# Kernel tuning notes

Hardware: AMD Instinct MI355X
Metric: run time of the kernel (lower is better)

## Reference

```python
import jax, jax.numpy as jnp
import numpy as np

DIM = 1024
NUM_HEADS = 16
HEAD_DIM = DIM // NUM_HEADS
SCALE = 1.0 / float(np.sqrt(HEAD_DIM))


def setup_inputs() -> dict:
    key = jax.random.key(0)
    ks = jax.random.split(key, 5)
    B, S = 2, 2048
    x = jax.random.normal(ks[0], (B, S, DIM), dtype=jnp.float32)
    qkv_w = jax.random.normal(ks[1], (3 * DIM, DIM), dtype=jnp.float32) * (1.0 / np.sqrt(DIM))
    qkv_b = jax.random.normal(ks[2], (3 * DIM,), dtype=jnp.float32) * 0.02
    proj_w = jax.random.normal(ks[3], (DIM, DIM), dtype=jnp.float32) * (1.0 / np.sqrt(DIM))
    proj_b = jax.random.normal(ks[4], (DIM,), dtype=jnp.float32) * 0.02
    return {"x": x, "qkv_w": qkv_w, "qkv_b": qkv_b, "proj_w": proj_w, "proj_b": proj_b}


def reference(x, qkv_w, qkv_b, proj_w, proj_b):
    B, S, _ = x.shape
    # qkv projection: (B,S,3*DIM) -> (3, B, H, S, Dh)
    qkv = x @ qkv_w.T + qkv_b
    qkv = qkv.reshape(B, S, 3, NUM_HEADS, HEAD_DIM).transpose(2, 0, 3, 1, 4)
    q, k, v = qkv[0], qkv[1], qkv[2]
    # scaled dot-product attention (full score matrix, as in the original)
    scores = jnp.einsum('bhqd,bhkd->bhqk', q, k) * SCALE
    attn = jax.nn.softmax(scores, axis=-1)
    out = jnp.einsum('bhqk,bhkd->bhqd', attn, v)  # (B,H,S,Dh)
    out = out.transpose(0, 2, 1, 3).reshape(B, S, DIM)
    return out @ proj_w.T + proj_b
```

## Files before the change

kernel.cpp:

```cpp
#include <hip/hip_runtime.h>

#define DIM_ 1024
#define NH_ 16
#define HD_ 64
#define B_ 2
#define S_ 2048
#define M_ (B_ * S_)
#define NQKV_ (3 * DIM_)

typedef __attribute__((ext_vector_type(8))) __bf16 bf16x8;
typedef __attribute__((ext_vector_type(4))) __bf16 bf16x4;
typedef __attribute__((ext_vector_type(4))) float f32x4;

__device__ __forceinline__ void gl_lds16(const void* g, void* l) {
  __builtin_amdgcn_global_load_lds(
      (__attribute__((address_space(1))) void*)const_cast<void*>(g),
      (__attribute__((address_space(3))) void*)l, 16, 0, 0);
}

#define N4_X 1048576
#define N4_W1 786432
#define N4_W2 262144
__global__ __launch_bounds__(256) void cast_all(const float* __restrict__ x,
                                                const float* __restrict__ w1,
                                                const float* __restrict__ w2,
                                                __bf16* __restrict__ xb,
                                                __bf16* __restrict__ w1b,
                                                __bf16* __restrict__ w2b) {
  int i = blockIdx.x * 256 + threadIdx.x;
  const int stride = gridDim.x * 256;
  for (; i < N4_X + N4_W1 + N4_W2; i += stride) {
    const float4* src;
    bf16x4* dst;
    int j;
    if (i < N4_X) { src = (const float4*)x; dst = (bf16x4*)xb; j = i; }
    else if (i < N4_X + N4_W1) { src = (const float4*)w1; dst = (bf16x4*)w1b; j = i - N4_X; }
    else { src = (const float4*)w2; dst = (bf16x4*)w2b; j = i - (N4_X + N4_W1); }
    float4 v = src[j];
    bf16x4 o;
    o[0] = (__bf16)v.x; o[1] = (__bf16)v.y; o[2] = (__bf16)v.z; o[3] = (__bf16)v.w;
    dst[j] = o;
  }
}

template <int MODE, int BM>
__global__ __launch_bounds__(512, 4) void gemm_bt(const __bf16* __restrict__ A,
                                                  const __bf16* __restrict__ Bw,
                                                  const float* __restrict__ bias,
                                                  __bf16* __restrict__ Qp, __bf16* __restrict__ Kp,
                                                  __bf16* __restrict__ Vt,
                                                  float* __restrict__ Cout) {
  constexpr int KD = 1024;
  constexpr int BN = 128;
  constexpr int MT = BM / 64;
  constexpr int NC = (BM + BN) / 64;
  __shared__ __bf16 As[BM * 64];
  __shared__ __bf16 Bs[BN * 64];
  const int tid = threadIdx.x;
  const int lane = tid & 63;
  const int wave = tid >> 6;
  const int quad = lane >> 4;
  const int r16 = lane & 15;
  const int wm = wave >> 1;
  const int wn = wave & 1;
  const int m0 = blockIdx.y * BM;
  const int n0 = blockIdx.x * BN;

  const f32x4 fz = {0.f, 0.f, 0.f, 0.f};
  f32x4 acc[MT][4];
#pragma unroll
  for (int i = 0; i < MT; ++i)
#pragma unroll
    for (int j = 0; j < 4; ++j) acc[i][j] = fz;

  const __bf16* gp[NC];
  __bf16* lp[NC];
#pragma unroll
  for (int i = 0; i < NC; ++i) {
    const int c = tid + i * 512;
    if (c < BM * 8) {
      const int r = c >> 3, cc = c & 7;
      gp[i] = A + (size_t)(m0 + r) * KD + ((cc ^ (r & 7)) * 8);
      lp[i] = &As[c * 8];
    } else {
      const int c2 = c - BM * 8;
      const int r = c2 >> 3, cc = c2 & 7;
      gp[i] = Bw + (size_t)(n0 + r) * KD + ((cc ^ (r & 7)) * 8);
      lp[i] = &Bs[c2 * 8];
    }
  }

  for (int kt = 0; kt < KD / 64; ++kt) {
    __syncthreads();
#pragma unroll
    for (int i = 0; i < NC; ++i) { gl_lds16(gp[i], lp[i]); gp[i] += 64; }
    __syncthreads();

#pragma unroll
    for (int sub = 0; sub < 2; ++sub) {
      const int ch = ((sub * 4 + quad) ^ (r16 & 7)) * 8;
      bf16x8 af[MT], bfr[4];
#pragma unroll
      for (int mt = 0; mt < MT; ++mt)
        af[mt] = *(const bf16x8*)&As[(wm * MT * 16 + mt * 16 + r16) * 64 + ch];
#pragma unroll
      for (int nt = 0; nt < 4; ++nt)
        bfr[nt] = *(const bf16x8*)&Bs[(wn * 64 + nt * 16 + r16) * 64 + ch];
#pragma unroll
      for (int mt = 0; mt < MT; ++mt)
#pragma unroll
        for (int nt = 0; nt < 4; ++nt)
          acc[mt][nt] =
              __builtin_amdgcn_mfma_f32_16x16x32_bf16(af[mt], bfr[nt], acc[mt][nt], 0, 0, 0);
    }
  }

  if (MODE == 0) {
#pragma unroll
    for (int nt = 0; nt < 4; ++nt) {
      const int n = n0 + wn * 64 + nt * 16 + r16;
      const int sel = n >> 10;
      const int h = (n >> 6) & 15;
      const int dh = n & 63;
      const float bs = bias[n];
      if (sel == 2) {
#pragma unroll
        for (int mt = 0; mt < MT; ++mt) {
          const int m = m0 + wm * MT * 16 + mt * 16 + quad * 4;
          const int b = m >> 11;
          const int s = m & 2047;
          const int slot = (s & ~31) | (((s >> 2) & 3) << 3) | (((s >> 4) & 1) << 2);
          bf16x4 ov;
#pragma unroll
          for (int r = 0; r < 4; ++r) ov[r] = (__bf16)(acc[mt][nt][r] + bs);
          *(bf16x4*)&Vt[((size_t)((b * NH_ + h) * HD_ + dh)) * S_ + slot] = ov;
        }
      } else {
        __bf16* dst = (sel == 0) ? Qp : Kp;
        const float mul = (sel == 0) ? 0.18033688011112042f : 1.0f;
#pragma unroll
        for (int mt = 0; mt < MT; ++mt) {
#pragma unroll
          for (int r = 0; r < 4; ++r) {
            const int m = m0 + wm * MT * 16 + mt * 16 + quad * 4 + r;
            const int b = m >> 11;
            const int s = m & 2047;
            dst[((size_t)((b * NH_ + h) * S_ + s)) * HD_ + dh] =
                (__bf16)((acc[mt][nt][r] + bs) * mul);
          }
        }
      }
    }
  } else {
#pragma unroll
    for (int nt = 0; nt < 4; ++nt) {
      const int n = n0 + wn * 64 + nt * 16 + r16;
      const float bs = bias[n];
#pragma unroll
      for (int mt = 0; mt < MT; ++mt) {
#pragma unroll
        for (int r = 0; r < 4; ++r) {
          const int m = m0 + wm * MT * 16 + mt * 16 + quad * 4 + r;
          Cout[(size_t)m * DIM_ + n] = acc[mt][nt][r] + bs;
        }
      }
    }
  }
}

__global__ __launch_bounds__(512, 4) void attn(const __bf16* __restrict__ Qp,
                                               const __bf16* __restrict__ Kp,
                                               const __bf16* __restrict__ Vtp,
                                               __bf16* __restrict__ ctx) {
  __shared__ __bf16 smem[2][2][2][64 * 64];
  const int tid = threadIdx.x;
  const int lane = tid & 63;
  const int wave = tid >> 6;
  const int quad = lane >> 4;
  const int r16 = lane & 15;
  const int qg = wave & 3;
  const int kh = wave >> 2;
  const int bh = blockIdx.y;
  const int q0 = blockIdx.x * 128;

  bf16x8 qf[2][2];
#pragma unroll
  for (int g = 0; g < 2; ++g) {
    const __bf16* qb = Qp + ((size_t)bh * S_ + q0 + qg * 32 + g * 16 + r16) * HD_;
    qf[g][0] = *(const bf16x8*)(qb + quad * 8);
    qf[g][1] = *(const bf16x8*)(qb + 32 + quad * 8);
  }

  const f32x4 fz = {0.f, 0.f, 0.f, 0.f};
  f32x4 o[2][4];
  float lsum[2] = {0.f, 0.f};
#pragma unroll
  for (int g = 0; g < 2; ++g)
#pragma unroll
    for (int d = 0; d < 4; ++d) o[g][d] = fz;

  const __bf16* gp[4];
  int gstep[4], lkv[4], lhh[4], lof[4];
#pragma unroll
  for (int i = 0; i < 4; ++i) {
    const int c = tid + i * 512;
    if (c < 1024) {
      const int hh = c >> 9, c2 = c & 511;
      const int kr = c2 >> 3, kc = c2 & 7;
      gp[i] = Kp + ((size_t)bh * S_ + hh * 1024 + kr) * HD_ + ((kc ^ (kr & 7)) * 8);
      gstep[i] = 64 * HD_;
      lkv[i] = 0; lhh[i] = hh; lof[i] = c2 * 8;
    } else {
      const int c1 = c - 1024;
      const int hh = c1 >> 9, c2 = c1 & 511;
      const int vr = c2 >> 3, vc = c2 & 7;
      gp[i] = Vtp + ((size_t)bh * HD_ + vr) * S_ + hh * 1024 + ((vc ^ (vr & 7)) * 8);
      gstep[i] = 64;
      lkv[i] = 1; lhh[i] = hh; lof[i] = c2 * 8;
    }
  }

#pragma unroll
  for (int i = 0; i < 4; ++i) {
    gl_lds16(gp[i], &smem[0][lkv[i]][lhh[i]][lof[i]]);
    gp[i] += gstep[i];
  }

  for (int kt = 0; kt < 16; ++kt) {
    const int cb = kt & 1;
    __syncthreads();
    if (kt + 1 < 16) {
#pragma unroll
      for (int i = 0; i < 4; ++i) {
        gl_lds16(gp[i], &smem[cb ^ 1][lkv[i]][lhh[i]][lof[i]]);
        gp[i] += gstep[i];
      }
    }

    const __bf16* Kt = &smem[cb][0][kh][0];
    const __bf16* Vt2 = &smem[cb][1][kh][0];
#pragma unroll
    for (int ks = 0; ks < 2; ++ks) {
      f32x4 sa[2][2];
#pragma unroll
      for (int mt2 = 0; mt2 < 2; ++mt2) {
        const int row = (ks * 2 + mt2) * 16 + r16;
        bf16x8 k0 = *(const bf16x8*)&Kt[row * 64 + ((quad ^ (row & 7)) * 8)];
        bf16x8 k1 = *(const bf16x8*)&Kt[row * 64 + (((4 + quad) ^ (row & 7)) * 8)];
#pragma unroll
        for (int g = 0; g < 2; ++g) {
          f32x4 t = fz;
          t = __builtin_amdgcn_mfma_f32_16x16x32_bf16(k0, qf[g][0], t, 0, 0, 0);
          t = __builtin_amdgcn_mfma_f32_16x16x32_bf16(k1, qf[g][1], t, 0, 0, 0);
          sa[mt2][g] = t;
        }
      }

      bf16x8 pf[2];
#pragma unroll
      for (int g = 0; g < 2; ++g)
#pragma unroll
        for (int r = 0; r < 4; ++r) {
          float p0 = __builtin_amdgcn_exp2f(sa[0][g][r]);
          float p1 = __builtin_amdgcn_exp2f(sa[1][g][r]);
          lsum[g] += p0 + p1;
          pf[g][r] = (__bf16)p0;
          pf[g][4 + r] = (__bf16)p1;
        }

#pragma unroll
      for (int dt = 0; dt < 4; ++dt) {
        const int row = dt * 16 + r16;
        bf16x8 va = *(const bf16x8*)&Vt2[row * 64 + (((ks * 4 + quad) ^ (row & 7)) * 8)];
#pragma unroll
        for (int g = 0; g < 2; ++g)
          o[g][dt] = __builtin_amdgcn_mfma_f32_16x16x32_bf16(va, pf[g], o[g][dt], 0, 0, 0);
      }
    }
  }

#pragma unroll
  for (int g = 0; g < 2; ++g) {
    lsum[g] += __shfl_xor(lsum[g], 16);
    lsum[g] += __shfl_xor(lsum[g], 32);
  }

  float* xch = (float*)smem;
  __syncthreads();
  if (kh == 1) {
#pragma unroll
    for (int g = 0; g < 2; ++g) {
#pragma unroll
      for (int dt = 0; dt < 4; ++dt)
        *(f32x4*)&xch[(qg * 8 + g * 4 + dt) * 256 + lane * 4] = o[g][dt];
      xch[8192 + qg * 128 + g * 64 + lane] = lsum[g];
    }
  }
  __syncthreads();
  if (kh == 0) {
    const int b = bh >> 4, h = bh & 15;
#pragma unroll
    for (int g = 0; g < 2; ++g) {
      const float l = lsum[g] + xch[8192 + qg * 128 + g * 64 + lane];
      const float inv = 1.0f / l;
      const int s = q0 + qg * 32 + g * 16 + r16;
#pragma unroll
      for (int dt = 0; dt < 4; ++dt) {
        f32x4 op = *(const f32x4*)&xch[(qg * 8 + g * 4 + dt) * 256 + lane * 4];
        bf16x4 ov;
#pragma unroll
        for (int r = 0; r < 4; ++r) ov[r] = (__bf16)((o[g][dt][r] + op[r]) * inv);
        *(bf16x4*)&ctx[((size_t)(b * S_ + s)) * DIM_ + h * 64 + dt * 16 + quad * 4] = ov;
      }
    }
  }
}

extern "C" void kernel_launch(void* const* d_in, const int* in_sizes, int n_in, void* d_out,
                              int out_size, void* d_ws, size_t ws_size, hipStream_t stream) {
  const float* x = (const float*)d_in[0];
  const float* qkv_w = (const float*)d_in[1];
  const float* qkv_b = (const float*)d_in[2];
  const float* proj_w = (const float*)d_in[3];
  const float* proj_b = (const float*)d_in[4];
  float* out = (float*)d_out;

  char* ws = (char*)d_ws;
  __bf16* Xb = (__bf16*)(ws);
  __bf16* Wb = (__bf16*)(ws + 8388608);
  __bf16* Pb = (__bf16*)(ws + 14680064);
  __bf16* Qp = (__bf16*)(ws + 16777216);
  __bf16* Kp = (__bf16*)(ws + 25165824);
  __bf16* Vt = (__bf16*)(ws + 33554432);
  __bf16* Cx = (__bf16*)(ws + 41943040);

  cast_all<<<2048, 256, 0, stream>>>(x, qkv_w, proj_w, Xb, Wb, Pb);
  gemm_bt<0, 128><<<dim3(NQKV_ / 128, M_ / 128), 512, 0, stream>>>(Xb, Wb, qkv_b, Qp, Kp, Vt,
                                                                   nullptr);
  attn<<<dim3(S_ / 128, 32), 512, 0, stream>>>(Qp, Kp, Vt, Cx);
  gemm_bt<1, 64><<<dim3(DIM_ / 128, M_ / 64), 512, 0, stream>>>(Cx, Pb, proj_b, nullptr, nullptr,
                                                                nullptr, out);
}
```

Measured before the change: 173.9 us.

## Split attention keys across four wave groups with 1024-thread blocks

The attention kernel now runs 1024 threads per block. Four key-split wave groups each handle 32 keys of a 128-key tile, and partial outputs are combined through a two-stage LDS reduction. The grid is reordered so that blockIdx.x indexes batch-head, which changes the block scheduling order and possibly L2 reuse. The aim is to cut the serial loop work per wave and the global-to-LDS load count per thread. The cost is a larger 70 KB LDS footprint, fewer resident blocks per CU, and extra reduction synchronisation.

```diff
diff --git a/kernel.cpp b/kernel.cpp
--- a/kernel.cpp
+++ b/kernel.cpp
@@ -168,11 +168,16 @@
   }
 }
 
-__global__ __launch_bounds__(512, 4) void attn(const __bf16* __restrict__ Qp,
-                                               const __bf16* __restrict__ Kp,
-                                               const __bf16* __restrict__ Vtp,
-                                               __bf16* __restrict__ ctx) {
-  __shared__ __bf16 smem[2][2][2][64 * 64];
+__global__ __launch_bounds__(1024, 8) void attn(const __bf16* __restrict__ Qp,
+                                                const __bf16* __restrict__ Kp,
+                                                const __bf16* __restrict__ Vtp,
+                                                __bf16* __restrict__ ctx) {
+  __shared__ __align__(16) char smem_raw[71680];
+  __bf16* Ks = (__bf16*)smem_raw;
+  __bf16* Vs = (__bf16*)(smem_raw + 32768);
+  float* xch = (float*)smem_raw;
+  float* lx = (float*)(smem_raw + 69632);
+
   const int tid = threadIdx.x;
   const int lane = tid & 63;
   const int wave = tid >> 6;
@@ -180,8 +185,8 @@
   const int r16 = lane & 15;
   const int qg = wave & 3;
   const int kh = wave >> 2;
-  const int bh = blockIdx.y;
-  const int q0 = blockIdx.x * 128;
+  const int bh = blockIdx.x;
+  const int q0 = blockIdx.y * 128;
 
   bf16x8 qf[2][2];
 #pragma unroll
@@ -199,83 +204,60 @@
 #pragma unroll
     for (int d = 0; d < 4; ++d) o[g][d] = fz;
 
-  const __bf16* gp[4];
-  int gstep[4], lkv[4], lhh[4], lof[4];
-#pragma unroll
-  for (int i = 0; i < 4; ++i) {
-    const int c = tid + i * 512;
-    if (c < 1024) {
-      const int hh = c >> 9, c2 = c & 511;
-      const int kr = c2 >> 3, kc = c2 & 7;
-      gp[i] = Kp + ((size_t)bh * S_ + hh * 1024 + kr) * HD_ + ((kc ^ (kr & 7)) * 8);
-      gstep[i] = 64 * HD_;
-      lkv[i] = 0; lhh[i] = hh; lof[i] = c2 * 8;
-    } else {
-      const int c1 = c - 1024;
-      const int hh = c1 >> 9, c2 = c1 & 511;
-      const int vr = c2 >> 3, vc = c2 & 7;
-      gp[i] = Vtp + ((size_t)bh * HD_ + vr) * S_ + hh * 1024 + ((vc ^ (vr & 7)) * 8);
-      gstep[i] = 64;
-      lkv[i] = 1; lhh[i] = hh; lof[i] = c2 * 8;
-    }
-  }
-
-#pragma unroll
-  for (int i = 0; i < 4; ++i) {
-    gl_lds16(gp[i], &smem[0][lkv[i]][lhh[i]][lof[i]]);
-    gp[i] += gstep[i];
-  }
+  const int krow = tid >> 3, kcol = tid & 7;
+  const __bf16* gk = Kp + ((size_t)bh * S_ + krow) * HD_ + ((kcol ^ (krow & 7)) * 8);
+  const int kof = tid * 8;
+  const int vrow = tid >> 4, vcol = tid & 15;
+  const __bf16* gv = Vtp + ((size_t)bh * HD_ + vrow) * S_ + ((vcol ^ (vrow & 15)) * 8);
+  const int vof = tid * 8;
+
+  gl_lds16(gk, &Ks[kof]); gk += 128 * HD_;
+  gl_lds16(gv, &Vs[vof]); gv += 128;
 
   for (int kt = 0; kt < 16; ++kt) {
     const int cb = kt & 1;
     __syncthreads();
     if (kt + 1 < 16) {
-#pragma unroll
-      for (int i = 0; i < 4; ++i) {
-        gl_lds16(gp[i], &smem[cb ^ 1][lkv[i]][lhh[i]][lof[i]]);
-        gp[i] += gstep[i];
-      }
-    }
-
-    const __bf16* Kt = &smem[cb][0][kh][0];
-    const __bf16* Vt2 = &smem[cb][1][kh][0];
-#pragma unroll
-    for (int ks = 0; ks < 2; ++ks) {
-      f32x4 sa[2][2];
-#pragma unroll
-      for (int mt2 = 0; mt2 < 2; ++mt2) {
-        const int row = (ks * 2 + mt2) * 16 + r16;
-        bf16x8 k0 = *(const bf16x8*)&Kt[row * 64 + ((quad ^ (row & 7)) * 8)];
-        bf16x8 k1 = *(const bf16x8*)&Kt[row * 64 + (((4 + quad) ^ (row & 7)) * 8)];
-#pragma unroll
-        for (int g = 0; g < 2; ++g) {
-          f32x4 t = fz;
-          t = __builtin_amdgcn_mfma_f32_16x16x32_bf16(k0, qf[g][0], t, 0, 0, 0);
-          t = __builtin_amdgcn_mfma_f32_16x16x32_bf16(k1, qf[g][1], t, 0, 0, 0);
-          sa[mt2][g] = t;
-        }
-      }
-
-      bf16x8 pf[2];
+      gl_lds16(gk, &Ks[(cb ^ 1) * 8192 + kof]); gk += 128 * HD_;
+      gl_lds16(gv, &Vs[(cb ^ 1) * 8192 + vof]); gv += 128;
+    }
+    const __bf16* Kt = &Ks[cb * 8192];
+    const __bf16* Vt2 = &Vs[cb * 8192];
+
+    f32x4 sa[2][2];
+#pragma unroll
+    for (int mt2 = 0; mt2 < 2; ++mt2) {
+      const int row = kh * 32 + mt2 * 16 + r16;
+      bf16x8 k0 = *(const bf16x8*)&Kt[row * 64 + ((quad ^ (row & 7)) * 8)];
+      bf16x8 k1 = *(const bf16x8*)&Kt[row * 64 + (((4 + quad) ^ (row & 7)) * 8)];
+#pragma unroll
+      for (int g = 0; g < 2; ++g) {
+        f32x4 t = fz;
+        t = __builtin_amdgcn_mfma_f32_16x16x32_bf16(k0, qf[g][0], t, 0, 0, 0);
+        t = __builtin_amdgcn_mfma_f32_16x16x32_bf16(k1, qf[g][1], t, 0, 0, 0);
+        sa[mt2][g] = t;
+      }
+    }
+
+    bf16x8 pf[2];
+#pragma unroll
+    for (int g = 0; g < 2; ++g)
+#pragma unroll
+      for (int r = 0; r < 4; ++r) {
+        float p0 = __builtin_amdgcn_exp2f(sa[0][g][r]);
+        float p1 = __builtin_amdgcn_exp2f(sa[1][g][r]);
+        lsum[g] += p0 + p1;
+        pf[g][r] = (__bf16)p0;
+        pf[g][4 + r] = (__bf16)p1;
+      }
+
+#pragma unroll
+    for (int dt = 0; dt < 4; ++dt) {
+      const int row = dt * 16 + r16;
+      bf16x8 va = *(const bf16x8*)&Vt2[row * 128 + (((kh * 4 + quad) ^ (row & 15)) * 8)];
 #pragma unroll
       for (int g = 0; g < 2; ++g)
-#pragma unroll
-        for (int r = 0; r < 4; ++r) {
-          float p0 = __builtin_amdgcn_exp2f(sa[0][g][r]);
-          float p1 = __builtin_amdgcn_exp2f(sa[1][g][r]);
-          lsum[g] += p0 + p1;
-          pf[g][r] = (__bf16)p0;
-          pf[g][4 + r] = (__bf16)p1;
-        }
-
-#pragma unroll
-      for (int dt = 0; dt < 4; ++dt) {
-        const int row = dt * 16 + r16;
-        bf16x8 va = *(const bf16x8*)&Vt2[row * 64 + (((ks * 4 + quad) ^ (row & 7)) * 8)];
-#pragma unroll
-        for (int g = 0; g < 2; ++g)
-          o[g][dt] = __builtin_amdgcn_mfma_f32_16x16x32_bf16(va, pf[g], o[g][dt], 0, 0, 0);
-      }
+        o[g][dt] = __builtin_amdgcn_mfma_f32_16x16x32_bf16(va, pf[g], o[g][dt], 0, 0, 0);
     }
   }
 
@@ -285,31 +267,53 @@
     lsum[g] += __shfl_xor(lsum[g], 32);
   }
 
-  float* xch = (float*)smem;
+  __syncthreads();
+  if (quad == 0)
+#pragma unroll
+    for (int g = 0; g < 2; ++g) lx[kh * 128 + qg * 32 + g * 16 + r16] = lsum[g];
+  if (kh >= 2) {
+    float* dst = xch + (kh - 2) * 8704;
+#pragma unroll
+    for (int g = 0; g < 2; ++g)
+#pragma unroll
+      for (int dt = 0; dt < 4; ++dt)
+        *(f32x4*)&dst[(qg * 32 + g * 16 + r16) * 68 + dt * 16 + quad * 4] = o[g][dt];
+  }
+  __syncthreads();
+  if (kh < 2) {
+    const float* src = xch + kh * 8704;
+#pragma unroll
+    for (int g = 0; g < 2; ++g)
+#pragma unroll
+      for (int dt = 0; dt < 4; ++dt) {
+        f32x4 p = *(const f32x4*)&src[(qg * 32 + g * 16 + r16) * 68 + dt * 16 + quad * 4];
+#pragma unroll
+        for (int r = 0; r < 4; ++r) o[g][dt][r] += p[r];
+      }
+  }
   __syncthreads();
   if (kh == 1) {
 #pragma unroll
-    for (int g = 0; g < 2; ++g) {
+    for (int g = 0; g < 2; ++g)
 #pragma unroll
       for (int dt = 0; dt < 4; ++dt)
-        *(f32x4*)&xch[(qg * 8 + g * 4 + dt) * 256 + lane * 4] = o[g][dt];
-      xch[8192 + qg * 128 + g * 64 + lane] = lsum[g];
-    }
+        *(f32x4*)&xch[(qg * 32 + g * 16 + r16) * 68 + dt * 16 + quad * 4] = o[g][dt];
   }
   __syncthreads();
   if (kh == 0) {
     const int b = bh >> 4, h = bh & 15;
 #pragma unroll
     for (int g = 0; g < 2; ++g) {
-      const float l = lsum[g] + xch[8192 + qg * 128 + g * 64 + lane];
+      const int q = qg * 32 + g * 16 + r16;
+      const float l = lsum[g] + lx[128 + q] + lx[256 + q] + lx[384 + q];
       const float inv = 1.0f / l;
-      const int s = q0 + qg * 32 + g * 16 + r16;
+      const int s = q0 + q;
 #pragma unroll
       for (int dt = 0; dt < 4; ++dt) {
-        f32x4 op = *(const f32x4*)&xch[(qg * 8 + g * 4 + dt) * 256 + lane * 4];
+        f32x4 p = *(const f32x4*)&xch[q * 68 + dt * 16 + quad * 4];
         bf16x4 ov;
 #pragma unroll
-        for (int r = 0; r < 4; ++r) ov[r] = (__bf16)((o[g][dt][r] + op[r]) * inv);
+        for (int r = 0; r < 4; ++r) ov[r] = (__bf16)((o[g][dt][r] + p[r]) * inv);
         *(bf16x4*)&ctx[((size_t)(b * S_ + s)) * DIM_ + h * 64 + dt * 16 + quad * 4] = ov;
       }
     }
@@ -337,7 +341,7 @@
   cast_all<<<2048, 256, 0, stream>>>(x, qkv_w, proj_w, Xb, Wb, Pb);
   gemm_bt<0, 128><<<dim3(NQKV_ / 128, M_ / 128), 512, 0, stream>>>(Xb, Wb, qkv_b, Qp, Kp, Vt,
                                                                    nullptr);
-  attn<<<dim3(S_ / 128, 32), 512, 0, stream>>>(Qp, Kp, Vt, Cx);
+  attn<<<dim3(32, S_ / 128), 1024, 0, stream>>>(Qp, Kp, Vt, Cx);
   gemm_bt<1, 64><<<dim3(DIM_ / 128, M_ / 64), 512, 0, stream>>>(Cx, Pb, proj_b, nullptr, nullptr,
                                                                 nullptr, out);
 }
```

Result: slower. 371.1 us (+113.4%).
